# Performance work log

Measured on AMD Instinct MI355X. Metric: run time of the kernel, lower is better.

The kernel has to match this reference:

```python
import jax, jax.numpy as jnp
import numpy as np

DIM = 64
D = DIM // 2
COND_DIM = 64
HIDDEN = 512
N_BINS = 8
TAIL = 3.0
MIN_BW = 1e-3
MIN_BH = 1e-3
MIN_DER = 1e-3
MAX_DER = 10.0
EPS = 1e-6
BATCH = 131072


def _pad_left_zero(x):
    # pad last axis with one leading zero
    pads = [(0, 0)] * (x.ndim - 1) + [(1, 0)]
    return jnp.pad(x, pads)


def rq_spline_forward(inputs, widths, heights, derivatives):
    # inputs: [B, D2]; widths/heights: [B, D2, K]; derivatives: [B, D2, K+1]
    num_bins = widths.shape[-1]
    left, right = -TAIL, TAIL
    bottom, top = -TAIL, TAIL

    w = jax.nn.softmax(widths, axis=-1) * (right - left - MIN_BW * num_bins) + MIN_BW
    cumw = _pad_left_zero(jnp.cumsum(w, axis=-1)) + left          # [B, D2, K+1]
    w = cumw[..., 1:] - cumw[..., :-1]

    h = jax.nn.softmax(heights, axis=-1) * (top - bottom - MIN_BH * num_bins) + MIN_BH
    cumh = _pad_left_zero(jnp.cumsum(h, axis=-1)) + bottom        # [B, D2, K+1]
    h = cumh[..., 1:] - cumh[..., :-1]

    der = jnp.minimum(jax.nn.softplus(derivatives) + MIN_DER, MAX_DER)  # [B, D2, K+1]

    inside = (inputs >= left) & (inputs <= right)
    x = jnp.clip(inputs, left, right)

    # data-dependent bin search
    bin_idx = jnp.sum((x[..., None] >= cumw[..., 1:]).astype(jnp.int32), axis=-1)
    bin_idx = jnp.clip(bin_idx, 0, num_bins - 1)

    def gth(t):
        return jnp.take_along_axis(t, bin_idx[..., None], axis=-1)[..., 0]

    in_cumw = gth(cumw[..., :-1] if False else cumw)  # cumwidths gather uses same idx
    in_cumw = gth(cumw)
    in_bw = jnp.maximum(gth(w), EPS)
    out_cumh = gth(cumh)
    out_bh = gth(h)
    delta = out_bh / in_bw
    d_left = gth(der[..., :-1])
    d_right = gth(der[..., 1:])

    theta = (x - in_cumw) / in_bw
    tomt = theta * (1.0 - theta)
    numer = out_bh * (delta * theta**2 + d_left * tomt)
    denom = jnp.maximum(delta + (d_left + d_right - 2.0 * delta) * tomt, EPS)
    out_inside = out_cumh + numer / denom

    der_num = delta**2 * (d_right * theta**2 + 2.0 * delta * tomt + d_left * (1.0 - theta) ** 2)
    der_den = denom**2
    der_num = jnp.maximum(der_num, EPS)
    der_den = jnp.maximum(der_den, EPS)
    lad_inside = jnp.log(der_num) - jnp.log(der_den) - jnp.log(in_bw)

    outputs = jnp.where(inside, out_inside, inputs)
    logabsdet = jnp.where(inside, lad_inside, 0.0)

    outputs = jnp.nan_to_num(outputs, nan=0.0, posinf=TAIL, neginf=-TAIL)
    logabsdet = jnp.nan_to_num(logabsdet, nan=0.0, posinf=0.0, neginf=0.0)
    return outputs, logabsdet


def setup_inputs() -> dict:
    key = jax.random.key(0)
    ks = jax.random.split(key, 8)
    in_dim = D + COND_DIM
    out_dim = (DIM - D) * (3 * N_BINS + 1)
    s1 = 1.0 / np.sqrt(in_dim)
    s2 = 1.0 / np.sqrt(HIDDEN)
    return {
        "z": jax.random.normal(ks[0], (BATCH, DIM), jnp.float32),
        "condition": jax.random.normal(ks[1], (BATCH, COND_DIM), jnp.float32),
        "W1": jax.random.normal(ks[2], (in_dim, HIDDEN), jnp.float32) * s1,
        "b1": jnp.zeros((HIDDEN,), jnp.float32),
        "W2": jax.random.normal(ks[3], (HIDDEN, HIDDEN), jnp.float32) * s2,
        "b2": jnp.zeros((HIDDEN,), jnp.float32),
        "W3": jax.random.normal(ks[4], (HIDDEN, out_dim), jnp.float32) * s2,
        "b3": jnp.zeros((out_dim,), jnp.float32),
    }


def reference(z, condition, W1, b1, W2, b2, W3, b3):
    z1, z2 = z[:, :D], z[:, D:]
    x = jnp.concatenate([z1, condition], axis=1)
    hdd = jax.nn.relu(x @ W1 + b1)
    hdd = jax.nn.relu(hdd @ W2 + b2)
    params = hdd @ W3 + b3                                   # [B, (DIM-D)*(3K+1)]
    params = params.reshape(params.shape[0], DIM - D, 3 * N_BINS + 1)
    widths = params[..., :N_BINS]
    heights = params[..., N_BINS:2 * N_BINS]
    derivs = params[..., 2 * N_BINS:]
    z2_new, logabsdet = rq_spline_forward(z2, widths, heights, derivs)
    log_det = jnp.sum(logabsdet, axis=1)
    return jnp.concatenate([z1, z2_new], axis=1), log_det
```

## Files before the change

### kernel.cpp

```cpp
#include <hip/hip_runtime.h>
#include <hip/hip_fp16.h>


typedef _Float16 f16x8 __attribute__((ext_vector_type(8)));
typedef float f32x4 __attribute__((ext_vector_type(4)));

#define MROWS 32
#define XS 104
#define TPB 512

#define OFF_H1 0
#define OFF_L1 49152
#define OFF_H2 98304
#define OFF_L2 360448
#define OFF_H3 622592
#define OFF_L3 1032192

#define SMEM_BYTES 78848

__global__ __launch_bounds__(256) void prep_weights(
    const float* __restrict__ W1, const float* __restrict__ W2,
    const float* __restrict__ W3, _Float16* __restrict__ ws)
{
  int idx = blockIdx.x * 256 + threadIdx.x;
  float v; int hoff, loff;
  if (idx < 49152) {
    int n = idx / 96, k = idx - n * 96;
    v = W1[k * 512 + n];
    hoff = OFF_H1 + idx; loff = OFF_L1 + idx;
  } else if (idx < 311296) {
    int i = idx - 49152;
    int n = i >> 9, k = i & 511;
    v = W2[k * 512 + n];
    hoff = OFF_H2 + i; loff = OFF_L2 + i;
  } else if (idx < 720896) {
    int i = idx - 311296;
    int n = i >> 9, k = i & 511;
    v = W3[k * 800 + n];
    hoff = OFF_H3 + i; loff = OFF_L3 + i;
  } else {
    return;
  }
  _Float16 hi = (_Float16)v;
  _Float16 lo = (_Float16)(v - (float)hi);
  ws[hoff] = hi; ws[loff] = lo;
}

__device__ __forceinline__ void mfma3(f32x4& c, f16x8 aH, f16x8 aL, f16x8 bH, f16x8 bL) {
  c = __builtin_amdgcn_mfma_f32_16x16x32_f16(aH, bH, c, 0, 0, 0);
  c = __builtin_amdgcn_mfma_f32_16x16x32_f16(aL, bH, c, 0, 0, 0);
  c = __builtin_amdgcn_mfma_f32_16x16x32_f16(aH, bL, c, 0, 0, 0);
}

__device__ __forceinline__ int swz(int row, int col) {
  return row * 512 + ((((col >> 3) ^ (row & 7)) << 3) | (col & 7));
}

__global__ __launch_bounds__(TPB, 2) void fused_flow(
    const float* __restrict__ z, const float* __restrict__ cond,
    const float* __restrict__ b1, const float* __restrict__ b2,
    const float* __restrict__ b3, const _Float16* __restrict__ ws,
    float* __restrict__ out, int B)
{
  extern __shared__ char smem[];
  _Float16* hbH = (_Float16*)(smem);
  _Float16* hbL = (_Float16*)(smem + 32768);
  _Float16* xH  = (_Float16*)(smem + 65536);
  _Float16* xL  = (_Float16*)(smem + 72192);
  float* pbuf   = (float*)(smem);

  const int tid  = threadIdx.x;
  const int lane = tid & 63;
  const int wave = tid >> 6;
  const int r15  = lane & 15;
  const int g4   = lane >> 4;
  const int row0 = blockIdx.x * MROWS;

  const _Float16* w1H = ws + OFF_H1; const _Float16* w1L = ws + OFF_L1;
  const _Float16* w2H = ws + OFF_H2; const _Float16* w2L = ws + OFF_L2;
  const _Float16* w3H = ws + OFF_H3; const _Float16* w3L = ws + OFF_L3;

  #pragma unroll
  for (int rep = 0; rep < 2; ++rep) {
    int i = tid + rep * TPB;
    int r = i >> 5, c = i & 31;
    out[(row0 + r) * 64 + c] = z[(row0 + r) * 64 + c];
  }

  #pragma unroll
  for (int rep = 0; rep < 6; ++rep) {
    int i = tid + rep * TPB;
    int r = i / 96, c = i - r * 96;
    float v = (c < 32) ? z[(row0 + r) * 64 + c] : cond[(row0 + r) * 64 + (c - 32)];
    _Float16 hi = (_Float16)v;
    xH[r * XS + c] = hi;
    xL[r * XS + c] = (_Float16)(v - (float)hi);
  }
  __syncthreads();

  f32x4 acc[2][4];
  #pragma unroll
  for (int mt = 0; mt < 2; ++mt)
    #pragma unroll
    for (int t = 0; t < 4; ++t)
      acc[mt][t] = (f32x4){0.f, 0.f, 0.f, 0.f};

  #pragma unroll
  for (int ks = 0; ks < 3; ++ks) {
    int kb = ks * 32 + g4 * 8;
    f16x8 a0H = *(const f16x8*)(xH + r15 * XS + kb);
    f16x8 a0L = *(const f16x8*)(xL + r15 * XS + kb);
    f16x8 a1H = *(const f16x8*)(xH + (r15 + 16) * XS + kb);
    f16x8 a1L = *(const f16x8*)(xL + (r15 + 16) * XS + kb);
    #pragma unroll
    for (int t = 0; t < 4; ++t) {
      int ncol = (wave * 4 + t) * 16 + r15;
      f16x8 bH = *(const f16x8*)(w1H + ncol * 96 + kb);
      f16x8 bL = *(const f16x8*)(w1L + ncol * 96 + kb);
      mfma3(acc[0][t], a0H, a0L, bH, bL);
      mfma3(acc[1][t], a1H, a1L, bH, bL);
    }
  }
  #pragma unroll
  for (int t = 0; t < 4; ++t) {
    int ncol = (wave * 4 + t) * 16 + r15;
    float bias = b1[ncol];
    #pragma unroll
    for (int mt = 0; mt < 2; ++mt)
      #pragma unroll
      for (int i = 0; i < 4; ++i) {
        int row = mt * 16 + g4 * 4 + i;
        float v = fmaxf(acc[mt][t][i] + bias, 0.f);
        _Float16 hi = (_Float16)v;
        int off = swz(row, ncol);
        hbH[off] = hi;
        hbL[off] = (_Float16)(v - (float)hi);
      }
  }
  __syncthreads();

  #pragma unroll
  for (int mt = 0; mt < 2; ++mt)
    #pragma unroll
    for (int t = 0; t < 4; ++t)
      acc[mt][t] = (f32x4){0.f, 0.f, 0.f, 0.f};

  for (int ks = 0; ks < 16; ++ks) {
    int kb = ks * 32 + g4 * 8;
    int g = kb >> 3;
    int o0 = r15 * 512 + (((g ^ (r15 & 7)) << 3));
    int o1 = (r15 + 16) * 512 + (((g ^ (r15 & 7)) << 3));
    f16x8 a0H = *(const f16x8*)(hbH + o0);
    f16x8 a0L = *(const f16x8*)(hbL + o0);
    f16x8 a1H = *(const f16x8*)(hbH + o1);
    f16x8 a1L = *(const f16x8*)(hbL + o1);
    #pragma unroll
    for (int t = 0; t < 4; ++t) {
      int ncol = (wave * 4 + t) * 16 + r15;
      f16x8 bH = *(const f16x8*)(w2H + ncol * 512 + kb);
      f16x8 bL = *(const f16x8*)(w2L + ncol * 512 + kb);
      mfma3(acc[0][t], a0H, a0L, bH, bL);
      mfma3(acc[1][t], a1H, a1L, bH, bL);
    }
  }
  __syncthreads();
  #pragma unroll
  for (int t = 0; t < 4; ++t) {
    int ncol = (wave * 4 + t) * 16 + r15;
    float bias = b2[ncol];
    #pragma unroll
    for (int mt = 0; mt < 2; ++mt)
      #pragma unroll
      for (int i = 0; i < 4; ++i) {
        int row = mt * 16 + g4 * 4 + i;
        float v = fmaxf(acc[mt][t][i] + bias, 0.f);
        _Float16 hi = (_Float16)v;
        int off = swz(row, ncol);
        hbH[off] = hi;
        hbL[off] = (_Float16)(v - (float)hi);
      }
  }
  __syncthreads();

  f32x4 acc3[2][7];
  #pragma unroll
  for (int mt = 0; mt < 2; ++mt)
    #pragma unroll
    for (int tt = 0; tt < 7; ++tt)
      acc3[mt][tt] = (f32x4){0.f, 0.f, 0.f, 0.f};

  for (int ks = 0; ks < 16; ++ks) {
    int kb = ks * 32 + g4 * 8;
    int g = kb >> 3;
    int o0 = r15 * 512 + (((g ^ (r15 & 7)) << 3));
    int o1 = (r15 + 16) * 512 + (((g ^ (r15 & 7)) << 3));
    f16x8 a0H = *(const f16x8*)(hbH + o0);
    f16x8 a0L = *(const f16x8*)(hbL + o0);
    f16x8 a1H = *(const f16x8*)(hbH + o1);
    f16x8 a1L = *(const f16x8*)(hbL + o1);
    #pragma unroll
    for (int tt = 0; tt < 7; ++tt) {
      int nt = wave + tt * 8;
      if (nt < 50) {
        int ncol = nt * 16 + r15;
        f16x8 bH = *(const f16x8*)(w3H + ncol * 512 + kb);
        f16x8 bL = *(const f16x8*)(w3L + ncol * 512 + kb);
        mfma3(acc3[0][tt], a0H, a0L, bH, bL);
        mfma3(acc3[1][tt], a1H, a1L, bH, bL);
      }
    }
  }

  float logdet_part = 0.f;
  const int sr  = tid >> 4;
  const int sdl = tid & 15;

  #pragma unroll 1
  for (int c = 0; c < 2; ++c) {
    __syncthreads();
    #pragma unroll
    for (int tt = 0; tt < 7; ++tt) {
      int nt = wave + tt * 8;
      if (nt >= c * 25 && nt < c * 25 + 25) {
        int ncolg = nt * 16 + r15;
        int ncoll = ncolg - c * 400;
        float bias = b3[ncolg];
        #pragma unroll
        for (int mt = 0; mt < 2; ++mt)
          #pragma unroll
          for (int i = 0; i < 4; ++i) {
            int row = mt * 16 + g4 * 4 + i;
            pbuf[row * 401 + ncoll] = acc3[mt][tt][i] + bias;
          }
      }
    }
    __syncthreads();

    {
      int dim = c * 16 + sdl;
      float p[25];
      #pragma unroll
      for (int j = 0; j < 25; ++j) p[j] = pbuf[sr * 401 + sdl * 25 + j];

      float cw[9], ch[9], dv[9];
      {
        float m = p[0];
        #pragma unroll
        for (int j = 1; j < 8; ++j) m = fmaxf(m, p[j]);
        float e[8]; float s = 0.f;
        #pragma unroll
        for (int j = 0; j < 8; ++j) { e[j] = __expf(p[j] - m); s += e[j]; }
        float inv = 5.992f / s;
        cw[0] = -3.f; float a = 0.f;
        #pragma unroll
        for (int j = 0; j < 8; ++j) { a += e[j] * inv + 0.001f; cw[j + 1] = a - 3.f; }
      }
      {
        float m = p[8];
        #pragma unroll
        for (int j = 1; j < 8; ++j) m = fmaxf(m, p[8 + j]);
        float e[8]; float s = 0.f;
        #pragma unroll
        for (int j = 0; j < 8; ++j) { e[j] = __expf(p[8 + j] - m); s += e[j]; }
        float inv = 5.992f / s;
        ch[0] = -3.f; float a = 0.f;
        #pragma unroll
        for (int j = 0; j < 8; ++j) { a += e[j] * inv + 0.001f; ch[j + 1] = a - 3.f; }
      }
      #pragma unroll
      for (int j = 0; j < 9; ++j) {
        float t = p[16 + j];
        float sp = fmaxf(t, 0.f) + log1pf(__expf(-fabsf(t)));
        dv[j] = fminf(sp + 0.001f, 10.f);
      }

      float xin = z[(row0 + sr) * 64 + 32 + dim];
      bool inside = (xin >= -3.f) && (xin <= 3.f);
      float xc = fminf(fmaxf(xin, -3.f), 3.f);
      int b = 0;
      #pragma unroll
      for (int j = 1; j <= 8; ++j) b += (xc >= cw[j]) ? 1 : 0;
      if (b > 7) b = 7;

      float icw = cw[0], icw1 = cw[1], och = ch[0], och1 = ch[1], dl0 = dv[0], dr0 = dv[1];
      #pragma unroll
      for (int j = 1; j < 8; ++j) {
        bool sel = (b == j);
        icw  = sel ? cw[j]     : icw;
        icw1 = sel ? cw[j + 1] : icw1;
        och  = sel ? ch[j]     : och;
        och1 = sel ? ch[j + 1] : och1;
        dl0  = sel ? dv[j]     : dl0;
        dr0  = sel ? dv[j + 1] : dr0;
      }
      float ibw   = fmaxf(icw1 - icw, 1e-6f);
      float obh   = och1 - och;
      float delta = obh / ibw;
      float th    = (xc - icw) / ibw;
      float om    = 1.f - th;
      float tomt  = th * om;
      float numer = obh * (delta * th * th + dl0 * tomt);
      float denom = fmaxf(delta + (dl0 + dr0 - 2.f * delta) * tomt, 1e-6f);
      float outi  = och + numer / denom;
      float dn    = delta * delta * (dr0 * th * th + 2.f * delta * tomt + dl0 * om * om);
      float dd    = denom * denom;
      dn = fmaxf(dn, 1e-6f); dd = fmaxf(dd, 1e-6f);
      float lad   = __logf(dn) - __logf(dd) - __logf(ibw);

      float outv = inside ? outi : xin;
      float ladv = inside ? lad : 0.f;

      out[(row0 + sr) * 64 + 32 + dim] = outv;

      float s = ladv;
      s += __shfl_xor(s, 1);
      s += __shfl_xor(s, 2);
      s += __shfl_xor(s, 4);
      s += __shfl_xor(s, 8);
      if (sdl == 0) logdet_part += s;
    }
  }
  if (sdl == 0) out[(size_t)B * 64 + row0 + sr] = logdet_part;
}

extern "C" void kernel_launch(void* const* d_in, const int* in_sizes, int n_in,
                              void* d_out, int out_size, void* d_ws, size_t ws_size,
                              hipStream_t stream) {
  const float* z    = (const float*)d_in[0];
  const float* cnd  = (const float*)d_in[1];
  const float* W1   = (const float*)d_in[2];
  const float* b1   = (const float*)d_in[3];
  const float* W2   = (const float*)d_in[4];
  const float* b2   = (const float*)d_in[5];
  const float* W3   = (const float*)d_in[6];
  const float* b3   = (const float*)d_in[7];
  float* out        = (float*)d_out;
  _Float16* ws      = (_Float16*)d_ws;

  int B = in_sizes[0] / 64;

  hipFuncSetAttribute((const void*)fused_flow,
                      hipFuncAttributeMaxDynamicSharedMemorySize, SMEM_BYTES);

  prep_weights<<<(720896 + 255) / 256, 256, 0, stream>>>(W1, W2, W3, ws);
  fused_flow<<<B / MROWS, TPB, SMEM_BYTES, stream>>>(z, cnd, b1, b2, b3, ws, out, B);
}
```

Measured before the change: 1.556 ms.

## Prefetch weight fragments and restructure layer-3 GEMM per spline chunk

```diff
diff --git a/kernel.cpp b/kernel.cpp
--- a/kernel.cpp
+++ b/kernel.cpp
@@ -16,7 +16,8 @@
 #define OFF_H3 622592
 #define OFF_L3 1032192
 
-#define SMEM_BYTES 78848
+#define PBUF_OFF 78848
+#define SMEM_BYTES 130176
 
 __global__ __launch_bounds__(256) void prep_weights(
     const float* __restrict__ W1, const float* __restrict__ W2,
@@ -56,7 +57,7 @@
   return row * 512 + ((((col >> 3) ^ (row & 7)) << 3) | (col & 7));
 }
 
-__global__ __launch_bounds__(TPB, 2) void fused_flow(
+__global__ __launch_bounds__(TPB, 1) void fused_flow(
     const float* __restrict__ z, const float* __restrict__ cond,
     const float* __restrict__ b1, const float* __restrict__ b2,
     const float* __restrict__ b3, const _Float16* __restrict__ ws,
@@ -67,7 +68,7 @@
   _Float16* hbL = (_Float16*)(smem + 32768);
   _Float16* xH  = (_Float16*)(smem + 65536);
   _Float16* xL  = (_Float16*)(smem + 72192);
-  float* pbuf   = (float*)(smem);
+  float* pbuf   = (float*)(smem + PBUF_OFF);
 
   const int tid  = threadIdx.x;
   const int lane = tid & 63;
@@ -145,22 +146,46 @@
     for (int t = 0; t < 4; ++t)
       acc[mt][t] = (f32x4){0.f, 0.f, 0.f, 0.f};
 
-  for (int ks = 0; ks < 16; ++ks) {
-    int kb = ks * 32 + g4 * 8;
-    int g = kb >> 3;
-    int o0 = r15 * 512 + (((g ^ (r15 & 7)) << 3));
-    int o1 = (r15 + 16) * 512 + (((g ^ (r15 & 7)) << 3));
-    f16x8 a0H = *(const f16x8*)(hbH + o0);
-    f16x8 a0L = *(const f16x8*)(hbL + o0);
-    f16x8 a1H = *(const f16x8*)(hbH + o1);
-    f16x8 a1L = *(const f16x8*)(hbL + o1);
+  {
+    const _Float16* pH[4]; const _Float16* pL[4];
     #pragma unroll
     for (int t = 0; t < 4; ++t) {
       int ncol = (wave * 4 + t) * 16 + r15;
-      f16x8 bH = *(const f16x8*)(w2H + ncol * 512 + kb);
-      f16x8 bL = *(const f16x8*)(w2L + ncol * 512 + kb);
-      mfma3(acc[0][t], a0H, a0L, bH, bL);
-      mfma3(acc[1][t], a1H, a1L, bH, bL);
+      pH[t] = w2H + ncol * 512 + g4 * 8;
+      pL[t] = w2L + ncol * 512 + g4 * 8;
+    }
+    f16x8 bch[4], bcl[4];
+    #pragma unroll
+    for (int t = 0; t < 4; ++t) {
+      bch[t] = *(const f16x8*)(pH[t]);
+      bcl[t] = *(const f16x8*)(pL[t]);
+    }
+    #pragma unroll
+    for (int ks = 0; ks < 16; ++ks) {
+      f16x8 bnh[4], bnl[4];
+      if (ks < 15) {
+        #pragma unroll
+        for (int t = 0; t < 4; ++t) {
+          bnh[t] = *(const f16x8*)(pH[t] + (ks + 1) * 32);
+          bnl[t] = *(const f16x8*)(pL[t] + (ks + 1) * 32);
+        }
+      }
+      int g = ks * 4 + g4;
+      int o0 = r15 * 512 + (((g ^ (r15 & 7)) << 3));
+      int o1 = (r15 + 16) * 512 + (((g ^ (r15 & 7)) << 3));
+      f16x8 a0H = *(const f16x8*)(hbH + o0);
+      f16x8 a0L = *(const f16x8*)(hbL + o0);
+      f16x8 a1H = *(const f16x8*)(hbH + o1);
+      f16x8 a1L = *(const f16x8*)(hbL + o1);
+      #pragma unroll
+      for (int t = 0; t < 4; ++t) {
+        mfma3(acc[0][t], a0H, a0L, bch[t], bcl[t]);
+        mfma3(acc[1][t], a1H, a1L, bch[t], bcl[t]);
+      }
+      if (ks < 15) {
+        #pragma unroll
+        for (int t = 0; t < 4; ++t) { bch[t] = bnh[t]; bcl[t] = bnl[t]; }
+      }
     }
   }
   __syncthreads();
@@ -182,56 +207,48 @@
   }
   __syncthreads();
 
-  f32x4 acc3[2][7];
-  #pragma unroll
-  for (int mt = 0; mt < 2; ++mt)
-    #pragma unroll
-    for (int tt = 0; tt < 7; ++tt)
-      acc3[mt][tt] = (f32x4){0.f, 0.f, 0.f, 0.f};
-
-  for (int ks = 0; ks < 16; ++ks) {
-    int kb = ks * 32 + g4 * 8;
-    int g = kb >> 3;
-    int o0 = r15 * 512 + (((g ^ (r15 & 7)) << 3));
-    int o1 = (r15 + 16) * 512 + (((g ^ (r15 & 7)) << 3));
-    f16x8 a0H = *(const f16x8*)(hbH + o0);
-    f16x8 a0L = *(const f16x8*)(hbL + o0);
-    f16x8 a1H = *(const f16x8*)(hbH + o1);
-    f16x8 a1L = *(const f16x8*)(hbL + o1);
-    #pragma unroll
-    for (int tt = 0; tt < 7; ++tt) {
-      int nt = wave + tt * 8;
-      if (nt < 50) {
-        int ncol = nt * 16 + r15;
-        f16x8 bH = *(const f16x8*)(w3H + ncol * 512 + kb);
-        f16x8 bL = *(const f16x8*)(w3L + ncol * 512 + kb);
-        mfma3(acc3[0][tt], a0H, a0L, bH, bL);
-        mfma3(acc3[1][tt], a1H, a1L, bH, bL);
-      }
-    }
-  }
-
   float logdet_part = 0.f;
   const int sr  = tid >> 4;
   const int sdl = tid & 15;
 
   #pragma unroll 1
   for (int c = 0; c < 2; ++c) {
-    __syncthreads();
-    #pragma unroll
-    for (int tt = 0; tt < 7; ++tt) {
-      int nt = wave + tt * 8;
-      if (nt >= c * 25 && nt < c * 25 + 25) {
+    #pragma unroll 1
+    for (int j = 0; j < 4; ++j) {
+      if (wave + 8 * j < 25) {
+        int nt = c * 25 + wave + 8 * j;
         int ncolg = nt * 16 + r15;
+        const _Float16* pH = w3H + ncolg * 512 + g4 * 8;
+        const _Float16* pL = w3L + ncolg * 512 + g4 * 8;
+        f32x4 acc0 = (f32x4){0.f, 0.f, 0.f, 0.f};
+        f32x4 acc1 = (f32x4){0.f, 0.f, 0.f, 0.f};
+        f16x8 bh = *(const f16x8*)(pH);
+        f16x8 bl = *(const f16x8*)(pL);
+        #pragma unroll
+        for (int ks = 0; ks < 16; ++ks) {
+          f16x8 bhn, bln;
+          if (ks < 15) {
+            bhn = *(const f16x8*)(pH + (ks + 1) * 32);
+            bln = *(const f16x8*)(pL + (ks + 1) * 32);
+          }
+          int g = ks * 4 + g4;
+          int o0 = r15 * 512 + (((g ^ (r15 & 7)) << 3));
+          int o1 = (r15 + 16) * 512 + (((g ^ (r15 & 7)) << 3));
+          f16x8 a0H = *(const f16x8*)(hbH + o0);
+          f16x8 a0L = *(const f16x8*)(hbL + o0);
+          f16x8 a1H = *(const f16x8*)(hbH + o1);
+          f16x8 a1L = *(const f16x8*)(hbL + o1);
+          mfma3(acc0, a0H, a0L, bh, bl);
+          mfma3(acc1, a1H, a1L, bh, bl);
+          if (ks < 15) { bh = bhn; bl = bln; }
+        }
         int ncoll = ncolg - c * 400;
         float bias = b3[ncolg];
         #pragma unroll
-        for (int mt = 0; mt < 2; ++mt)
-          #pragma unroll
-          for (int i = 0; i < 4; ++i) {
-            int row = mt * 16 + g4 * 4 + i;
-            pbuf[row * 401 + ncoll] = acc3[mt][tt][i] + bias;
-          }
+        for (int i = 0; i < 4; ++i) {
+          pbuf[(g4 * 4 + i) * 401 + ncoll]        = acc0[i] + bias;
+          pbuf[(16 + g4 * 4 + i) * 401 + ncoll]   = acc1[i] + bias;
+        }
       }
     }
     __syncthreads();
@@ -319,6 +336,7 @@
       s += __shfl_xor(s, 8);
       if (sdl == 0) logdet_part += s;
     }
+    __syncthreads();
   }
   if (sdl == 0) out[(size_t)B * 64 + row0 + sr] = logdet_part;
 }
```

After: 1.594 ms. 2.4% more time.
